# Kernel tuning notes

Hardware: AMD Instinct MI355X
Metric: run time of the kernel (lower is better)

Reference implementation:

```python
import jax, jax.numpy as jnp
import numpy as np

B, T, IN, H, L = 256, 512, 64, 128, 2

def _lstm_layer(x_tbi, w_ih, w_hh, b_ih, b_hh):
    # x_tbi: [T, B, in]; weights follow PyTorch layout: w_ih [4H, in], w_hh [4H, H]
    # Precompute input projections for all timesteps (one big GEMM).
    xg = jnp.einsum('tbi,gi->tbg', x_tbi, w_ih) + b_ih + b_hh  # [T, B, 4H]
    h0 = jnp.zeros((x_tbi.shape[1], w_hh.shape[1]), x_tbi.dtype)
    c0 = jnp.zeros_like(h0)
    def step(carry, xg_t):
        h, c = carry
        gates = xg_t + h @ w_hh.T  # [B, 4H]
        i, f, g, o = jnp.split(gates, 4, axis=-1)  # PyTorch gate order i,f,g,o
        i, f, o = jax.nn.sigmoid(i), jax.nn.sigmoid(f), jax.nn.sigmoid(o)
        c = f * c + i * jnp.tanh(g)
        h = o * jnp.tanh(c)
        return (h, c), h
    (_, _), hs = jax.lax.scan(step, (h0, c0), xg)
    return hs  # [T, B, H]

def setup_inputs() -> dict:
    key = jax.random.key(0)
    ks = jax.random.split(key, 12)
    s = 1.0 / np.sqrt(H)
    u = lambda k, shape: jax.random.uniform(k, shape, jnp.float32, -s, s)
    return {
        'x': jax.random.normal(ks[0], (B, T, IN), jnp.float32),
        'w_ih0': u(ks[1], (4 * H, IN)), 'w_hh0': u(ks[2], (4 * H, H)),
        'b_ih0': u(ks[3], (4 * H,)),   'b_hh0': u(ks[4], (4 * H,)),
        'w_ih1': u(ks[5], (4 * H, H)), 'w_hh1': u(ks[6], (4 * H, H)),
        'b_ih1': u(ks[7], (4 * H,)),   'b_hh1': u(ks[8], (4 * H,)),
        'fc_w': u(ks[9], (1, H)),      'fc_b': u(ks[10], (1,)),
    }

def reference(x, w_ih0, w_hh0, b_ih0, b_hh0, w_ih1, w_hh1, b_ih1, b_hh1, fc_w, fc_b):
    h = jnp.transpose(x, (1, 0, 2))  # [T, B, IN]
    h = _lstm_layer(h, w_ih0, w_hh0, b_ih0, b_hh0)
    h = _lstm_layer(h, w_ih1, w_hh1, b_ih1, b_hh1)
    last = h[-1]  # [B, H] == x[:, -1, :] in batch_first layout
    return last @ fc_w.T + fc_b  # [B, 1]
```

## Files before the change

### kernel.cpp

```cpp
#include <hip/hip_runtime.h>
#include <hip/hip_fp16.h>


#define TT 512
#define CH 16
#define NCH 32
#define MM (256 * 512)
#define HP 136

typedef _Float16 f16x2 __attribute__((ext_vector_type(2)));
typedef _Float16 f16x4 __attribute__((ext_vector_type(4)));
typedef _Float16 f16x8 __attribute__((ext_vector_type(8)));
typedef float f32x4 __attribute__((ext_vector_type(4)));

__device__ __forceinline__ float tanh_f(float x) {
    float e = __expf(2.0f * x);
    return 1.0f - 2.0f * __builtin_amdgcn_rcpf(e + 1.0f);
}
__device__ __forceinline__ float sigm_f(float x) {
    return __builtin_amdgcn_rcpf(1.0f + __expf(-x));
}

__global__ void cvt_f32_f16(const float* __restrict__ src,
                            _Float16* __restrict__ dst, int n4) {
    int i = blockIdx.x * blockDim.x + threadIdx.x;
    int stride = gridDim.x * blockDim.x;
    for (; i < n4; i += stride) {
        float4 v = ((const float4*)src)[i];
        f16x2 a; a.x = (_Float16)v.x; a.y = (_Float16)v.y;
        f16x2 b; b.x = (_Float16)v.z; b.y = (_Float16)v.w;
        ((f16x2*)dst)[2 * i]     = a;
        ((f16x2*)dst)[2 * i + 1] = b;
    }
}

__global__ __launch_bounds__(256, 1) void gemm_xg0(
    const float* __restrict__ A32, const _Float16* __restrict__ W,
    const float* __restrict__ bih, const float* __restrict__ bhh,
    _Float16* __restrict__ out)
{
    const int l  = threadIdx.x & 63;
    const int w  = threadIdx.x >> 6;
    const int mb = blockIdx.x * 64 + w * 16;
    const int c  = l & 15;
    const int q  = l >> 4;

    __shared__ float biasl[512];
    for (int i = threadIdx.x; i < 512; i += 256) biasl[i] = bih[i] + bhh[i];
    __syncthreads();

    f32x4 C[32];
    #pragma unroll
    for (int i = 0; i < 32; ++i) C[i] = (f32x4){0.f, 0.f, 0.f, 0.f};

    #pragma unroll
    for (int ks = 0; ks < 2; ++ks) {
        const float* ap = A32 + (size_t)(mb + c) * 64 + ks * 32 + q * 8;
        float4 v0 = ((const float4*)ap)[0];
        float4 v1 = ((const float4*)ap)[1];
        f16x8 Af;
        Af[0] = (_Float16)v0.x; Af[1] = (_Float16)v0.y;
        Af[2] = (_Float16)v0.z; Af[3] = (_Float16)v0.w;
        Af[4] = (_Float16)v1.x; Af[5] = (_Float16)v1.y;
        Af[6] = (_Float16)v1.z; Af[7] = (_Float16)v1.w;
        #pragma unroll
        for (int nt = 0; nt < 32; ++nt) {
            f16x8 Bf = *(const f16x8*)(W + (size_t)(nt * 16 + c) * 64 + ks * 32 + q * 8);
            C[nt] = __builtin_amdgcn_mfma_f32_16x16x32_f16(Af, Bf, C[nt], 0, 0, 0);
        }
    }
    #pragma unroll
    for (int uu = 0; uu < 8; ++uu) {
        float b0 = biasl[uu * 16 + c];
        float b1 = biasl[128 + uu * 16 + c];
        float b2 = biasl[256 + uu * 16 + c];
        float b3 = biasl[384 + uu * 16 + c];
        #pragma unroll
        for (int i = 0; i < 4; ++i) {
            int row = mb + q * 4 + i;
            f16x4 pk;
            pk[0] = (_Float16)(C[uu][i]      + b0);
            pk[1] = (_Float16)(C[8 + uu][i]  + b1);
            pk[2] = (_Float16)(C[16 + uu][i] + b2);
            pk[3] = (_Float16)(C[24 + uu][i] + b3);
            ((f16x4*)out)[(size_t)row * 128 + uu * 16 + c] = pk;
        }
    }
}

__global__ __launch_bounds__(512, 1) void lstm_fused(
    const float* __restrict__ whh0, const float* __restrict__ wih1,
    const float* __restrict__ whh1,
    const float* __restrict__ bih1, const float* __restrict__ bhh1,
    const _Float16* __restrict__ xg0,
    const float* __restrict__ fc_w, const float* __restrict__ fc_b,
    float* __restrict__ out)
{
    const int t = threadIdx.x;
    const int b = blockIdx.x;
    const int w = t >> 6;
    const int l = t & 63;
    const int q = l >> 4;
    const int c = l & 15;
    const int unit = (w << 4) + c;

    __shared__ __align__(16) _Float16 w1lds[512 * 128];
    __shared__ __align__(16) _Float16 h0tile[CH * HP];
    __shared__ __align__(16) _Float16 h1buf[2][128];
    __shared__ __align__(16) _Float16 xg1t[CH * 512];
    __shared__ float redbuf[128];

    {
        const int r = t;
        const float* src = wih1 + (size_t)r * 128;
        #pragma unroll
        for (int j = 0; j < 16; ++j) {
            float4 v0 = ((const float4*)src)[2 * j];
            float4 v1 = ((const float4*)src)[2 * j + 1];
            f16x8 f;
            f[0] = (_Float16)v0.x; f[1] = (_Float16)v0.y;
            f[2] = (_Float16)v0.z; f[3] = (_Float16)v0.w;
            f[4] = (_Float16)v1.x; f[5] = (_Float16)v1.y;
            f[6] = (_Float16)v1.z; f[7] = (_Float16)v1.w;
            *(f16x8*)&w1lds[r * 128 + ((j ^ (r & 7)) << 3)] = f;
        }
    }

    f16x8 B0[4][4], B1[4][4];
    #pragma unroll
    for (int g = 0; g < 4; ++g) {
        #pragma unroll
        for (int kt = 0; kt < 4; ++kt) {
            const size_t off = (size_t)((g << 7) + unit) * 128 + (kt << 5) + (q << 3);
            {
                float4 v0 = ((const float4*)(whh0 + off))[0];
                float4 v1 = ((const float4*)(whh0 + off))[1];
                f16x8 f;
                f[0] = (_Float16)v0.x; f[1] = (_Float16)v0.y;
                f[2] = (_Float16)v0.z; f[3] = (_Float16)v0.w;
                f[4] = (_Float16)v1.x; f[5] = (_Float16)v1.y;
                f[6] = (_Float16)v1.z; f[7] = (_Float16)v1.w;
                B0[g][kt] = f;
            }
            {
                float4 v0 = ((const float4*)(whh1 + off))[0];
                float4 v1 = ((const float4*)(whh1 + off))[1];
                f16x8 f;
                f[0] = (_Float16)v0.x; f[1] = (_Float16)v0.y;
                f[2] = (_Float16)v0.z; f[3] = (_Float16)v0.w;
                f[4] = (_Float16)v1.x; f[5] = (_Float16)v1.y;
                f[6] = (_Float16)v1.z; f[7] = (_Float16)v1.w;
                B1[g][kt] = f;
            }
        }
    }

    float bias1g[4];
    #pragma unroll
    for (int g = 0; g < 4; ++g)
        bias1g[g] = bih1[(g << 7) + unit] + bhh1[(g << 7) + unit];

    for (int i = t; i < CH * 512 / 8; i += 512)
        ((float4*)xg1t)[i] = make_float4(0.f, 0.f, 0.f, 0.f);
    if (t < 128) {
        h1buf[0][t] = (_Float16)0.f;
        h1buf[1][t] = (_Float16)0.f;
        h0tile[(CH - 1) * HP + t] = (_Float16)0.f;
    }

    const f16x4* __restrict__ xgp = (const f16x4*)xg0 + (size_t)b * TT * 128 + unit;
    f16x4 xr[4];
    xr[0] = xgp[0];
    xr[1] = xgp[128];
    xr[2] = xr[0]; xr[3] = xr[0];

    f32x4 a0[4], a1[4];
    #pragma unroll
    for (int g = 0; g < 4; ++g) {
        a0[g] = (f32x4){0.f, 0.f, 0.f, 0.f};
        a1[g] = (f32x4){0.f, 0.f, 0.f, 0.f};
    }

    float cst0 = 0.f, cst1 = 0.f;
    __syncthreads();

    #pragma unroll 1
    for (int k = 0; k <= NCH; ++k) {
        #pragma unroll
        for (int j = 0; j < CH; ++j) {
            const int rp = (j + CH - 1) & (CH - 1);

            f16x4 xv = xr[j & 3];
            f16x4 xg1v = *(const f16x4*)&xg1t[(j << 9) + (unit << 2)];
            #pragma unroll
            for (int g = 0; g < 4; ++g) {
                a0[g][0] = (float)xv[g];
                a1[g][0] = (float)xg1v[g];
            }
            xr[(j + 2) & 3] = xgp[(size_t)(k * CH + j + 2) * 128];

            #pragma unroll
            for (int kt = 0; kt < 4; ++kt) {
                f16x8 Af0 = *(const f16x8*)&h0tile[rp * HP + (kt << 5) + (q << 3)];
                f16x8 Af1 = *(const f16x8*)&h1buf[(j & 1) ^ 1][(kt << 5) + (q << 3)];
                #pragma unroll
                for (int g = 0; g < 4; ++g)
                    a0[g] = __builtin_amdgcn_mfma_f32_16x16x32_f16(Af0, B0[g][kt], a0[g], 0, 0, 0);
                #pragma unroll
                for (int g = 0; g < 4; ++g)
                    a1[g] = __builtin_amdgcn_mfma_f32_16x16x32_f16(Af1, B1[g][kt], a1[g], 0, 0, 0);
            }

            {
                float gi = sigm_f(a0[0][0]);
                float gf = sigm_f(a0[1][0]);
                float gg = tanh_f(a0[2][0]);
                float go = sigm_f(a0[3][0]);
                cst0 = gf * cst0 + gi * gg;
                float hh = go * tanh_f(cst0);
                if (l < 16) h0tile[j * HP + unit] = (_Float16)hh;
            }
            {
                float gi = sigm_f(a1[0][0]);
                float gf = sigm_f(a1[1][0]);
                float gg = tanh_f(a1[2][0]);
                float go = sigm_f(a1[3][0]);
                cst1 = gf * cst1 + gi * gg;
                float hh = go * tanh_f(cst1);
                if (l < 16) {
                    h1buf[j & 1][unit] = (_Float16)hh;
                    if (j == CH - 1) redbuf[unit] = hh;
                }
            }
            __syncthreads();
        }

        if (k < NCH) {
            f32x4 G[4];
            #pragma unroll
            for (int g = 0; g < 4; ++g)
                G[g] = (f32x4){bias1g[g], bias1g[g], bias1g[g], bias1g[g]};
            #pragma unroll
            for (int kt = 0; kt < 4; ++kt) {
                f16x8 Ag = *(const f16x8*)&h0tile[c * HP + (kt << 5) + (q << 3)];
                #pragma unroll
                for (int g = 0; g < 4; ++g) {
                    const int r = (g << 7) + unit;
                    f16x8 Bg = *(const f16x8*)&w1lds[r * 128 +
                                   ((((kt << 2) + q) ^ (c & 7)) << 3)];
                    G[g] = __builtin_amdgcn_mfma_f32_16x16x32_f16(Ag, Bg, G[g], 0, 0, 0);
                }
            }
            #pragma unroll
            for (int i2 = 0; i2 < 4; ++i2) {
                f16x4 pk;
                pk[0] = (_Float16)G[0][i2];
                pk[1] = (_Float16)G[1][i2];
                pk[2] = (_Float16)G[2][i2];
                pk[3] = (_Float16)G[3][i2];
                *(f16x4*)&xg1t[(((q << 2) + i2) << 9) + (unit << 2)] = pk;
            }
            __syncthreads();
        }
    }

    if (t < 64) {
        float p = redbuf[t] * fc_w[t] + redbuf[t + 64] * fc_w[t + 64];
        #pragma unroll
        for (int off = 32; off > 0; off >>= 1) p += __shfl_down(p, off, 64);
        if (t == 0) out[b] = p + fc_b[0];
    }
}

extern "C" void kernel_launch(void* const* d_in, const int* in_sizes, int n_in,
                              void* d_out, int out_size, void* d_ws, size_t ws_size,
                              hipStream_t stream) {
    const float* x     = (const float*)d_in[0];
    const float* w_ih0 = (const float*)d_in[1];
    const float* w_hh0 = (const float*)d_in[2];
    const float* b_ih0 = (const float*)d_in[3];
    const float* b_hh0 = (const float*)d_in[4];
    const float* w_ih1 = (const float*)d_in[5];
    const float* w_hh1 = (const float*)d_in[6];
    const float* b_ih1 = (const float*)d_in[7];
    const float* b_hh1 = (const float*)d_in[8];
    const float* fc_w  = (const float*)d_in[9];
    const float* fc_b  = (const float*)d_in[10];
    float* out = (float*)d_out;

    char* ws = (char*)d_ws;
    _Float16* xg    = (_Float16*)(ws);
    _Float16* w0_16 = (_Float16*)(ws + 134217728 + 65536);

    cvt_f32_f16<<<dim3(32), dim3(256), 0, stream>>>(w_ih0, w0_16, (512 * 64) / 4);

    gemm_xg0<<<dim3(MM / 64), dim3(256), 0, stream>>>(x, w0_16, b_ih0, b_hh0, xg);

    lstm_fused<<<dim3(256), dim3(512), 0, stream>>>(w_hh0, w_ih1, w_hh1,
                                                    b_ih1, b_hh1, xg,
                                                    fc_w, fc_b, out);
}
```

Before: 619.7 us.

## Fuse layer-0 input projection GEMM into recurrent LSTM kernel, halve chunk size

Removes the separate weight-convert and xg0 GEMM kernels. Each block now computes layer-0 input gates per chunk from x using register-resident W_ih0 fragments with MFMA, storing them in LDS next to the layer-1 input gates. This drops the global round trip through a 128 MB fp16 workspace and two kernel launches. In exchange, the per-chunk work in the serial kernel grows, and the chunk size is halved to 8 steps, which doubles the number of chunk-boundary phases and barriers.

```diff
diff --git a/kernel.cpp b/kernel.cpp
--- a/kernel.cpp
+++ b/kernel.cpp
@@ -3,12 +3,10 @@
 
 
 #define TT 512
-#define CH 16
-#define NCH 32
-#define MM (256 * 512)
+#define CH 8
+#define NCH 64
 #define HP 136
 
-typedef _Float16 f16x2 __attribute__((ext_vector_type(2)));
 typedef _Float16 f16x4 __attribute__((ext_vector_type(4)));
 typedef _Float16 f16x8 __attribute__((ext_vector_type(8)));
 typedef float f32x4 __attribute__((ext_vector_type(4)));
@@ -20,79 +18,21 @@
 __device__ __forceinline__ float sigm_f(float x) {
     return __builtin_amdgcn_rcpf(1.0f + __expf(-x));
 }
-
-__global__ void cvt_f32_f16(const float* __restrict__ src,
-                            _Float16* __restrict__ dst, int n4) {
-    int i = blockIdx.x * blockDim.x + threadIdx.x;
-    int stride = gridDim.x * blockDim.x;
-    for (; i < n4; i += stride) {
-        float4 v = ((const float4*)src)[i];
-        f16x2 a; a.x = (_Float16)v.x; a.y = (_Float16)v.y;
-        f16x2 b; b.x = (_Float16)v.z; b.y = (_Float16)v.w;
-        ((f16x2*)dst)[2 * i]     = a;
-        ((f16x2*)dst)[2 * i + 1] = b;
-    }
-}
-
-__global__ __launch_bounds__(256, 1) void gemm_xg0(
-    const float* __restrict__ A32, const _Float16* __restrict__ W,
-    const float* __restrict__ bih, const float* __restrict__ bhh,
-    _Float16* __restrict__ out)
-{
-    const int l  = threadIdx.x & 63;
-    const int w  = threadIdx.x >> 6;
-    const int mb = blockIdx.x * 64 + w * 16;
-    const int c  = l & 15;
-    const int q  = l >> 4;
-
-    __shared__ float biasl[512];
-    for (int i = threadIdx.x; i < 512; i += 256) biasl[i] = bih[i] + bhh[i];
-    __syncthreads();
-
-    f32x4 C[32];
-    #pragma unroll
-    for (int i = 0; i < 32; ++i) C[i] = (f32x4){0.f, 0.f, 0.f, 0.f};
-
-    #pragma unroll
-    for (int ks = 0; ks < 2; ++ks) {
-        const float* ap = A32 + (size_t)(mb + c) * 64 + ks * 32 + q * 8;
-        float4 v0 = ((const float4*)ap)[0];
-        float4 v1 = ((const float4*)ap)[1];
-        f16x8 Af;
-        Af[0] = (_Float16)v0.x; Af[1] = (_Float16)v0.y;
-        Af[2] = (_Float16)v0.z; Af[3] = (_Float16)v0.w;
-        Af[4] = (_Float16)v1.x; Af[5] = (_Float16)v1.y;
-        Af[6] = (_Float16)v1.z; Af[7] = (_Float16)v1.w;
-        #pragma unroll
-        for (int nt = 0; nt < 32; ++nt) {
-            f16x8 Bf = *(const f16x8*)(W + (size_t)(nt * 16 + c) * 64 + ks * 32 + q * 8);
-            C[nt] = __builtin_amdgcn_mfma_f32_16x16x32_f16(Af, Bf, C[nt], 0, 0, 0);
-        }
-    }
-    #pragma unroll
-    for (int uu = 0; uu < 8; ++uu) {
-        float b0 = biasl[uu * 16 + c];
-        float b1 = biasl[128 + uu * 16 + c];
-        float b2 = biasl[256 + uu * 16 + c];
-        float b3 = biasl[384 + uu * 16 + c];
-        #pragma unroll
-        for (int i = 0; i < 4; ++i) {
-            int row = mb + q * 4 + i;
-            f16x4 pk;
-            pk[0] = (_Float16)(C[uu][i]      + b0);
-            pk[1] = (_Float16)(C[8 + uu][i]  + b1);
-            pk[2] = (_Float16)(C[16 + uu][i] + b2);
-            pk[3] = (_Float16)(C[24 + uu][i] + b3);
-            ((f16x4*)out)[(size_t)row * 128 + uu * 16 + c] = pk;
-        }
-    }
-}
-
-__global__ __launch_bounds__(512, 1) void lstm_fused(
-    const float* __restrict__ whh0, const float* __restrict__ wih1,
-    const float* __restrict__ whh1,
+__device__ __forceinline__ f16x8 cvt8(float4 a, float4 b) {
+    f16x8 f;
+    f[0] = (_Float16)a.x; f[1] = (_Float16)a.y;
+    f[2] = (_Float16)a.z; f[3] = (_Float16)a.w;
+    f[4] = (_Float16)b.x; f[5] = (_Float16)b.y;
+    f[6] = (_Float16)b.z; f[7] = (_Float16)b.w;
+    return f;
+}
+
+__global__ __launch_bounds__(512, 1) void lstm_full(
+    const float* __restrict__ x,
+    const float* __restrict__ wih0, const float* __restrict__ whh0,
+    const float* __restrict__ bih0, const float* __restrict__ bhh0,
+    const float* __restrict__ wih1, const float* __restrict__ whh1,
     const float* __restrict__ bih1, const float* __restrict__ bhh1,
-    const _Float16* __restrict__ xg0,
     const float* __restrict__ fc_w, const float* __restrict__ fc_b,
     float* __restrict__ out)
 {
@@ -105,74 +45,108 @@
     const int unit = (w << 4) + c;
 
     __shared__ __align__(16) _Float16 w1lds[512 * 128];
+    __shared__ __align__(16) _Float16 xg0t[CH * 512];
+    __shared__ __align__(16) _Float16 xg1t[CH * 512];
     __shared__ __align__(16) _Float16 h0tile[CH * HP];
     __shared__ __align__(16) _Float16 h1buf[2][128];
-    __shared__ __align__(16) _Float16 xg1t[CH * 512];
     __shared__ float redbuf[128];
 
     {
         const int r = t;
         const float* src = wih1 + (size_t)r * 128;
         #pragma unroll
-        for (int j = 0; j < 16; ++j) {
-            float4 v0 = ((const float4*)src)[2 * j];
-            float4 v1 = ((const float4*)src)[2 * j + 1];
-            f16x8 f;
-            f[0] = (_Float16)v0.x; f[1] = (_Float16)v0.y;
-            f[2] = (_Float16)v0.z; f[3] = (_Float16)v0.w;
-            f[4] = (_Float16)v1.x; f[5] = (_Float16)v1.y;
-            f[6] = (_Float16)v1.z; f[7] = (_Float16)v1.w;
-            *(f16x8*)&w1lds[r * 128 + ((j ^ (r & 7)) << 3)] = f;
-        }
-    }
-
-    f16x8 B0[4][4], B1[4][4];
+        for (int j = 0; j < 16; ++j)
+            *(f16x8*)&w1lds[r * 128 + ((j ^ (r & 7)) << 3)] =
+                cvt8(((const float4*)src)[2 * j], ((const float4*)src)[2 * j + 1]);
+    }
+
+    f16x8 B0[4][4], B1[4][4], W0p[4][2];
     #pragma unroll
     for (int g = 0; g < 4; ++g) {
         #pragma unroll
         for (int kt = 0; kt < 4; ++kt) {
             const size_t off = (size_t)((g << 7) + unit) * 128 + (kt << 5) + (q << 3);
-            {
-                float4 v0 = ((const float4*)(whh0 + off))[0];
-                float4 v1 = ((const float4*)(whh0 + off))[1];
-                f16x8 f;
-                f[0] = (_Float16)v0.x; f[1] = (_Float16)v0.y;
-                f[2] = (_Float16)v0.z; f[3] = (_Float16)v0.w;
-                f[4] = (_Float16)v1.x; f[5] = (_Float16)v1.y;
-                f[6] = (_Float16)v1.z; f[7] = (_Float16)v1.w;
-                B0[g][kt] = f;
-            }
-            {
-                float4 v0 = ((const float4*)(whh1 + off))[0];
-                float4 v1 = ((const float4*)(whh1 + off))[1];
-                f16x8 f;
-                f[0] = (_Float16)v0.x; f[1] = (_Float16)v0.y;
-                f[2] = (_Float16)v0.z; f[3] = (_Float16)v0.w;
-                f[4] = (_Float16)v1.x; f[5] = (_Float16)v1.y;
-                f[6] = (_Float16)v1.z; f[7] = (_Float16)v1.w;
-                B1[g][kt] = f;
-            }
-        }
-    }
-
-    float bias1g[4];
+            B0[g][kt] = cvt8(((const float4*)(whh0 + off))[0],
+                             ((const float4*)(whh0 + off))[1]);
+            B1[g][kt] = cvt8(((const float4*)(whh1 + off))[0],
+                             ((const float4*)(whh1 + off))[1]);
+        }
+        #pragma unroll
+        for (int kt = 0; kt < 2; ++kt) {
+            const size_t off = (size_t)((g << 7) + unit) * 64 + (kt << 5) + (q << 3);
+            W0p[g][kt] = cvt8(((const float4*)(wih0 + off))[0],
+                              ((const float4*)(wih0 + off))[1]);
+        }
+    }
+    float bias0g[4], bias1g[4];
     #pragma unroll
-    for (int g = 0; g < 4; ++g)
+    for (int g = 0; g < 4; ++g) {
+        bias0g[g] = bih0[(g << 7) + unit] + bhh0[(g << 7) + unit];
         bias1g[g] = bih1[(g << 7) + unit] + bhh1[(g << 7) + unit];
-
-    for (int i = t; i < CH * 512 / 8; i += 512)
+    }
+
+    {
+        int i = t;
         ((float4*)xg1t)[i] = make_float4(0.f, 0.f, 0.f, 0.f);
+    }
     if (t < 128) {
         h1buf[0][t] = (_Float16)0.f;
         h1buf[1][t] = (_Float16)0.f;
         h0tile[(CH - 1) * HP + t] = (_Float16)0.f;
     }
 
-    const f16x4* __restrict__ xgp = (const f16x4*)xg0 + (size_t)b * TT * 128 + unit;
-    f16x4 xr[4];
-    xr[0] = xgp[0];
-    xr[1] = xgp[128];
-    xr[2] = xr[0]; xr[3] = xr[0];
+    float4 xs0, xs1, xs2, xs3;
+    auto load_x = [&](int base) {
+        const float* xp = x + ((size_t)b * TT + base + (c & 7)) * 64 + (q << 3);
+        xs0 = ((const float4*)xp)[0];
+        xs1 = ((const float4*)xp)[1];
+        xs2 = ((const float4*)(xp + 32))[0];
+        xs3 = ((const float4*)(xp + 32))[1];
+    };
+    auto xphase = [&]() {
+        f32x4 G[4];
+        #pragma unroll
+        for (int g = 0; g < 4; ++g)
+            G[g] = (f32x4){bias0g[g], bias0g[g], bias0g[g], bias0g[g]};
+        f16x8 Ax0 = cvt8(xs0, xs1);
+        f16x8 Ax1 = cvt8(xs2, xs3);
+        #pragma unroll
+        for (int g = 0; g < 4; ++g)
+            G[g] = __builtin_amdgcn_mfma_f32_16x16x32_f16(Ax0, W0p[g][0], G[g], 0, 0, 0);
+        #pragma unroll
+        for (int g = 0; g < 4; ++g)
+            G[g] = __builtin_amdgcn_mfma_f32_16x16x32_f16(Ax1, W0p[g][1], G[g], 0, 0, 0);
+        #pragma unroll
+        for (int i2 = 0; i2 < 4; ++i2) {
+            f16x4 pk;
+            pk[0] = (_Float16)G[0][i2]; pk[1] = (_Float16)G[1][i2];
+            pk[2] = (_Float16)G[2][i2]; pk[3] = (_Float16)G[3][i2];
+            *(f16x4*)&xg0t[((((q << 2) + i2) & 7) << 9) + (unit << 2)] = pk;
+        }
+    };
+    auto xgphase = [&]() {
+        f32x4 G[4];
+        #pragma unroll
+        for (int g = 0; g < 4; ++g)
+            G[g] = (f32x4){bias1g[g], bias1g[g], bias1g[g], bias1g[g]};
+        #pragma unroll
+        for (int kt = 0; kt < 4; ++kt) {
+            f16x8 Ah = *(const f16x8*)&h0tile[(c & 7) * HP + (kt << 5) + (q << 3)];
+            #pragma unroll
+            for (int g = 0; g < 4; ++g) {
+                f16x8 Bg = *(const f16x8*)&w1lds[(((g << 7) + unit) << 7) +
+                               ((((kt << 2) + q) ^ (c & 7)) << 3)];
+                G[g] = __builtin_amdgcn_mfma_f32_16x16x32_f16(Ah, Bg, G[g], 0, 0, 0);
+            }
+        }
+        #pragma unroll
+        for (int i2 = 0; i2 < 4; ++i2) {
+            f16x4 pk;
+            pk[0] = (_Float16)G[0][i2]; pk[1] = (_Float16)G[1][i2];
+            pk[2] = (_Float16)G[2][i2]; pk[3] = (_Float16)G[3][i2];
+            *(f16x4*)&xg1t[((((q << 2) + i2) & 7) << 9) + (unit << 2)] = pk;
+        }
+    };
 
     f32x4 a0[4], a1[4];
     #pragma unroll
@@ -180,25 +154,26 @@
         a0[g] = (f32x4){0.f, 0.f, 0.f, 0.f};
         a1[g] = (f32x4){0.f, 0.f, 0.f, 0.f};
     }
-
     float cst0 = 0.f, cst1 = 0.f;
+
+    load_x(0);
+    xphase();
     __syncthreads();
 
     #pragma unroll 1
     for (int k = 0; k <= NCH; ++k) {
+        if (k < NCH - 1) load_x((k + 1) * CH);
+
         #pragma unroll
         for (int j = 0; j < CH; ++j) {
             const int rp = (j + CH - 1) & (CH - 1);
-
-            f16x4 xv = xr[j & 3];
-            f16x4 xg1v = *(const f16x4*)&xg1t[(j << 9) + (unit << 2)];
+            f16x4 xv  = *(const f16x4*)&xg0t[(j << 9) + (unit << 2)];
+            f16x4 x1v = *(const f16x4*)&xg1t[(j << 9) + (unit << 2)];
             #pragma unroll
             for (int g = 0; g < 4; ++g) {
                 a0[g][0] = (float)xv[g];
-                a1[g][0] = (float)xg1v[g];
-            }
-            xr[(j + 2) & 3] = xgp[(size_t)(k * CH + j + 2) * 128];
-
+                a1[g][0] = (float)x1v[g];
+            }
             #pragma unroll
             for (int kt = 0; kt < 4; ++kt) {
                 f16x8 Af0 = *(const f16x8*)&h0tile[rp * HP + (kt << 5) + (q << 3)];
@@ -210,7 +185,6 @@
                 for (int g = 0; g < 4; ++g)
                     a1[g] = __builtin_amdgcn_mfma_f32_16x16x32_f16(Af1, B1[g][kt], a1[g], 0, 0, 0);
             }
-
             {
                 float gi = sigm_f(a0[0][0]);
                 float gf = sigm_f(a0[1][0]);
@@ -236,30 +210,8 @@
         }
 
         if (k < NCH) {
-            f32x4 G[4];
-            #pragma unroll
-            for (int g = 0; g < 4; ++g)
-                G[g] = (f32x4){bias1g[g], bias1g[g], bias1g[g], bias1g[g]};
-            #pragma unroll
-            for (int kt = 0; kt < 4; ++kt) {
-                f16x8 Ag = *(const f16x8*)&h0tile[c * HP + (kt << 5) + (q << 3)];
-                #pragma unroll
-                for (int g = 0; g < 4; ++g) {
-                    const int r = (g << 7) + unit;
-                    f16x8 Bg = *(const f16x8*)&w1lds[r * 128 +
-                                   ((((kt << 2) + q) ^ (c & 7)) << 3)];
-                    G[g] = __builtin_amdgcn_mfma_f32_16x16x32_f16(Ag, Bg, G[g], 0, 0, 0);
-                }
-            }
-            #pragma unroll
-            for (int i2 = 0; i2 < 4; ++i2) {
-                f16x4 pk;
-                pk[0] = (_Float16)G[0][i2];
-                pk[1] = (_Float16)G[1][i2];
-                pk[2] = (_Float16)G[2][i2];
-                pk[3] = (_Float16)G[3][i2];
-                *(f16x4*)&xg1t[(((q << 2) + i2) << 9) + (unit << 2)] = pk;
-            }
+            if (k < NCH - 1) xphase();
+            xgphase();
             __syncthreads();
         }
     }
@@ -287,16 +239,9 @@
     const float* fc_w  = (const float*)d_in[9];
     const float* fc_b  = (const float*)d_in[10];
     float* out = (float*)d_out;
-
-    char* ws = (char*)d_ws;
-    _Float16* xg    = (_Float16*)(ws);
-    _Float16* w0_16 = (_Float16*)(ws + 134217728 + 65536);
-
-    cvt_f32_f16<<<dim3(32), dim3(256), 0, stream>>>(w_ih0, w0_16, (512 * 64) / 4);
-
-    gemm_xg0<<<dim3(MM / 64), dim3(256), 0, stream>>>(x, w0_16, b_ih0, b_hh0, xg);
-
-    lstm_fused<<<dim3(256), dim3(512), 0, stream>>>(w_hh0, w_ih1, w_hh1,
-                                                    b_ih1, b_hh1, xg,
-                                                    fc_w, fc_b, out);
-}
+    (void)d_ws; (void)ws_size;
+
+    lstm_full<<<dim3(256), dim3(512), 0, stream>>>(
+        x, w_ih0, w_hh0, b_ih0, b_hh0,
+        w_ih1, w_hh1, b_ih1, b_hh1, fc_w, fc_b, out);
+}
```

Result: slower. 709.8 us (+14.5%).
